# Performance work log

Hardware: AMD Instinct MI355X
Metric: run time of the kernel (lower is better)

## Reference

```python
import jax, jax.numpy as jnp
import numpy as np

B, S, H = 8, 1024, 1024
NH, HD = 16, 64  # num heads, head dim


def _split_heads(x):
    # [B,S,H] -> [B,NH,S,HD]
    return x.reshape(B, S, NH, HD).transpose(0, 2, 1, 3)


def setup_inputs() -> dict:
    key = jax.random.key(0)
    ks = jax.random.split(key, 16)
    sc = 1.0 / np.sqrt(H)
    sch = 1.0 / np.sqrt(HD)
    return {
        "hidden_states": jax.random.normal(ks[0], (B, S, H), jnp.float32),
        "attention_mask": jnp.zeros((B, 1, 1, S), jnp.float32),
        "context_embedded": jax.random.normal(ks[1], (B, S, H), jnp.float32),
        "Wq": jax.random.normal(ks[2], (H, H), jnp.float32) * sc,
        "bq": jnp.zeros((H,), jnp.float32),
        "Wk": jax.random.normal(ks[3], (H, H), jnp.float32) * sc,
        "bk": jnp.zeros((H,), jnp.float32),
        "Wv": jax.random.normal(ks[4], (H, H), jnp.float32) * sc,
        "bv": jnp.zeros((H,), jnp.float32),
        "Wcq": jax.random.normal(ks[5], (HD, HD), jnp.float32) * sch,
        "bcq": jnp.zeros((HD,), jnp.float32),
        "Wck": jax.random.normal(ks[6], (HD, HD), jnp.float32) * sch,
        "bck": jnp.zeros((HD,), jnp.float32),
        "w_lqc": jax.random.normal(ks[7], (HD,), jnp.float32) * sch,
        "w_lqq": jax.random.normal(ks[8], (HD,), jnp.float32) * sch,
        "w_lkc": jax.random.normal(ks[9], (HD,), jnp.float32) * sch,
        "w_lkk": jax.random.normal(ks[10], (HD,), jnp.float32) * sch,
    }


def reference(hidden_states, attention_mask, context_embedded,
              Wq, bq, Wk, bk, Wv, bv, Wcq, bcq, Wck, bck,
              w_lqc, w_lqq, w_lkc, w_lkk):
    # projections -> [B,NH,S,HD]
    q = _split_heads(hidden_states @ Wq + bq)
    k = _split_heads(hidden_states @ Wk + bk)
    v = _split_heads(hidden_states @ Wv + bv)
    ce = _split_heads(context_embedded)

    # context gating for queries
    ce_q = ce @ Wcq + bcq
    lam_q = jax.nn.sigmoid(ce_q @ w_lqc[:, None] + q @ w_lqq[:, None])  # [B,NH,S,1]
    q_ctx = (1.0 - lam_q) * q + lam_q * ce_q

    # context gating for keys
    ce_k = ce @ Wck + bck
    lam_k = jax.nn.sigmoid(ce_k @ w_lkc[:, None] + k @ w_lkk[:, None])  # [B,NH,S,1]
    k_ctx = (1.0 - lam_k) * k + lam_k * ce_k

    scores = jnp.einsum("bhqd,bhkd->bhqk", q_ctx, k_ctx) / np.sqrt(HD)
    scores = scores + attention_mask
    probs = jax.nn.softmax(scores, axis=-1)
    ctx = jnp.einsum("bhqk,bhkd->bhqd", probs, v)
    return ctx.transpose(0, 2, 1, 3).reshape(B, S, H)
```

## Files before the change

kernel.cpp:

```cpp
#include <hip/hip_runtime.h>

typedef _Float16 f16;
typedef f16   f16x8 __attribute__((ext_vector_type(8)));
typedef f16   f16x4 __attribute__((ext_vector_type(4)));
typedef float f32x4 __attribute__((ext_vector_type(4)));

namespace {
constexpr int kB  = 8;
constexpr int kS  = 1024;
constexpr int kH  = 1024;
constexpr int kNH = 16;
constexpr int kHD = 64;
constexpr int kBH = kB * kNH;
constexpr int kRows = kBH * kS;
constexpr float kLog2e = 1.44269504088896f;
}

__device__ __forceinline__ float fast_exp2(float x) {
#if __has_builtin(__builtin_amdgcn_exp2f)
    return __builtin_amdgcn_exp2f(x);
#else
    return __expf(x * 0.693147180559945f);
#endif
}

__device__ __forceinline__ void async16(const f16* g, f16* l) {
    __builtin_amdgcn_global_load_lds(
        (const __attribute__((address_space(1))) unsigned int*)g,
        (__attribute__((address_space(3))) unsigned int*)l, 16, 0, 0);
}

__device__ __forceinline__ int phys4(int m, int c) {
    return ((m >> 1) << 3) | ((((m & 1) << 2) | c) ^ ((m >> 1) & 7));
}
__device__ __forceinline__ int phys8(int m, int c) {
    return (m << 3) | (c ^ (m & 7));
}

__global__ __launch_bounds__(256) void prep_all_kernel(
    const float* __restrict__ hs, const float* __restrict__ ce,
    const float* __restrict__ Wq, const float* __restrict__ Wk,
    const float* __restrict__ Wv, const float* __restrict__ Wcq,
    const float* __restrict__ Wck, const float* __restrict__ mask,
    f16* __restrict__ hs16, f16* __restrict__ ce16, f16* __restrict__ Wt,
    f16* __restrict__ Wct, unsigned int* __restrict__ kn,
    float* __restrict__ mm)
{
    const int id = blockIdx.x;
    const int t = threadIdx.x;
    __shared__ f16 T[64][72];
    __shared__ float red[4];

    if (id < 8192) {
        const int x = id & 4095, y = id >> 12;
        int i = (x * 256 + t) * 8;
        const float* src = y ? ce : hs;
        float4 a = *(const float4*)(src + i);
        float4 b = *(const float4*)(src + i + 4);
        union { f16 h[8]; uint4 u; } pk;
        pk.h[0] = (f16)a.x; pk.h[1] = (f16)a.y; pk.h[2] = (f16)a.z; pk.h[3] = (f16)a.w;
        pk.h[4] = (f16)b.x; pk.h[5] = (f16)b.y; pk.h[6] = (f16)b.z; pk.h[7] = (f16)b.w;
        if (y == 0) {
            *(uint4*)(hs16 + i) = pk.u;
        } else {
            int row = i >> 10, col = i & 1023;
            int bb = row >> 10, s = row & 1023;
            int h = col >> 6, d = col & 63;
            size_t o = ((((size_t)(bb * kNH + h) << 10) | s) << 6) | d;
            *(uint4*)(ce16 + o) = pk.u;
        }
    } else if (id < 8960) {
        const int tt = id - 8192;
        const int bx = tt & 15, by = (tt >> 4) & 15, bz = tt >> 8;
        const float* W = (bz == 0) ? Wq : (bz == 1) ? Wk : Wv;
        f16* out = Wt + (size_t)bz * kH * kH;
        const int k0 = by * 64, n0 = bx * 64;
#pragma unroll
        for (int i = 0; i < 4; ++i) {
            int idx = t + i * 256;
            int r = idx >> 4, cb = (idx & 15) * 4;
            float4 v = *(const float4*)(W + (size_t)(k0 + r) * kH + n0 + cb);
            T[cb + 0][r] = (f16)v.x; T[cb + 1][r] = (f16)v.y;
            T[cb + 2][r] = (f16)v.z; T[cb + 3][r] = (f16)v.w;
        }
        __syncthreads();
#pragma unroll
        for (int i = 0; i < 4; ++i) {
            int idx = t + i * 256;
            int r = idx >> 4, cb = (idx & 15) * 4;
            union { f16 h[4]; uint2 u; } pk;
#pragma unroll
            for (int j = 0; j < 4; ++j) pk.h[j] = T[r][cb + j];
            *(uint2*)(out + (size_t)(n0 + r) * kH + k0 + cb) = pk.u;
        }
    } else {
        const int bx = id - 8960;
        if (bx < 2) {
            const float* W = bx ? Wck : Wcq;
            f16* out = Wct + bx * kHD * kHD;
#pragma unroll
            for (int i = 0; i < 16; ++i) {
                int idx = i * 256 + t;
                int k = idx >> 6, n = idx & 63;
                out[n * 64 + k] = (f16)W[idx];
            }
            if (bx == 0 && t < kBH) kn[t] = 0u;
        } else {
            const int b = bx - 2;
            const float* mp = mask + b * kS;
            float v = fmaxf(fmaxf(mp[t], mp[t + 256]), fmaxf(mp[t + 512], mp[t + 768]));
#pragma unroll
            for (int off = 1; off < 64; off <<= 1) v = fmaxf(v, __shfl_xor(v, off, 64));
            if ((t & 63) == 0) red[t >> 6] = v;
            __syncthreads();
            if (t == 0) mm[b] = fmaxf(fmaxf(red[0], red[1]), fmaxf(red[2], red[3]));
        }
    }
}

__global__ __launch_bounds__(256, 3) void qkv_gemm_f16(
    const f16* __restrict__ hs16, const f16* __restrict__ Wt,
    const float* __restrict__ bq, const float* __restrict__ bk,
    const float* __restrict__ bv,
    f16* __restrict__ q16, f16* __restrict__ k16, f16* __restrict__ vt)
{
    const int z = blockIdx.z;
    const f16* Bmat = Wt + (size_t)z * kH * kH;
    const float* bias = (z == 0) ? bq : (z == 1) ? bk : bv;

    __shared__ f16 AB[2][2][128 * 32];

    const int tid = threadIdx.x;
    const int w = tid >> 6, lane = tid & 63;
    const int quad = lane >> 4, mh = lane & 15;
    const int wm = w >> 1, wn = w & 1;
    const int m0 = blockIdx.x * 128, n0 = blockIdx.y * 128;

    const f16* aptr[2];
#pragma unroll
    for (int i = 0; i < 2; ++i) {
        int P = (w * 2 + i) * 64 + lane;
        int r2 = P >> 3, s = P & 7;
        int bb = s ^ (r2 & 7);
        int m = (r2 << 1) | (bb >> 2), c = bb & 3;
        aptr[i] = hs16 + (size_t)(m0 + m) * kH + c * 8;
    }
    const ptrdiff_t bdelta = (Bmat + (size_t)n0 * kH) - (hs16 + (size_t)m0 * kH);

    auto issue = [&](int buf) {
#pragma unroll
        for (int i = 0; i < 2; ++i) {
            async16(aptr[i], AB[buf][0] + (w * 2 + i) * 512);
            async16(aptr[i] + bdelta, AB[buf][1] + (w * 2 + i) * 512);
            aptr[i] += 32;
        }
    };

    f32x4 acc[4][4];
#pragma unroll
    for (int i = 0; i < 4; ++i)
#pragma unroll
        for (int j = 0; j < 4; ++j) acc[i][j] = (f32x4){0.f, 0.f, 0.f, 0.f};

    const int aoff0 = phys4(wm * 64 + mh, quad) * 8;
    const int boff0 = phys4(wn * 64 + mh, quad) * 8;

    auto compute = [&](int buf) {
        f16x8 af[4], bf[4];
#pragma unroll
        for (int t = 0; t < 4; ++t)
            af[t] = *(const f16x8*)(AB[buf][0] + aoff0 + t * 512);
#pragma unroll
        for (int t = 0; t < 4; ++t)
            bf[t] = *(const f16x8*)(AB[buf][1] + boff0 + t * 512);
#pragma unroll
        for (int i = 0; i < 4; ++i)
#pragma unroll
            for (int j = 0; j < 4; ++j)
                acc[i][j] = __builtin_amdgcn_mfma_f32_16x16x32_f16(
                    af[i], bf[j], acc[i][j], 0, 0, 0);
    };

    issue(0);
    __syncthreads();

    for (int it = 0; it < 16; ++it) {
        issue(1);
        compute(0);
        __syncthreads();
        if (it < 15) issue(0);
        compute(1);
        __syncthreads();
    }

    if (z < 2) {
        f16* outp = (z == 0) ? q16 : k16;
        f16* Cb = &AB[0][0][0] + w * 1280;
        const int h    = (n0 + wn * 64) >> 6;
        const int bbb  = m0 >> 10;
        const int sb   = (m0 & 1023) + wm * 64;
        f16* base = outp + ((size_t)(bbb * kNH + h) * kS + sb) * kHD;
#pragma unroll
        for (int nt = 0; nt < 4; ++nt) {
            const float bn = bias[n0 + wn * 64 + nt * 16 + mh];
#pragma unroll
            for (int mt = 0; mt < 4; ++mt)
#pragma unroll
                for (int r = 0; r < 4; ++r)
                    Cb[(mt * 16 + quad * 4 + r) * 20 + mh] =
                        (f16)(acc[mt][nt][r] + bn);
#pragma unroll
            for (int p = 0; p < 4; ++p) {
                int row = (lane >> 2) + p * 16;
                int qtr = lane & 3;
                uint2 v = *(const uint2*)(&Cb[row * 20 + qtr * 4]);
                *(uint2*)(base + (size_t)row * kHD + nt * 16 + qtr * 4) = v;
            }
        }
    } else {
#pragma unroll
        for (int nt = 0; nt < 4; ++nt) {
            const int n = n0 + wn * 64 + nt * 16 + mh;
            const int h = n >> 6, d = n & 63;
            const float bn = bias[n];
#pragma unroll
            for (int mt = 0; mt < 4; ++mt) {
                int mbase = m0 + wm * 64 + mt * 16 + quad * 4;
                int bbb = mbase >> 10, s0 = mbase & 1023;
                union { f16 h4[4]; uint2 u; } pk;
#pragma unroll
                for (int r = 0; r < 4; ++r) pk.h4[r] = (f16)(acc[mt][nt][r] + bn);
                *(uint2*)(vt + ((size_t)(bbb * kNH + h) * kHD + d) * kS + s0) = pk.u;
            }
        }
    }
}

__global__ __launch_bounds__(256) void gate_mfma(
    const f16* __restrict__ ce16, const f16* __restrict__ Wct,
    const float* __restrict__ bcq, const float* __restrict__ bck,
    const float* __restrict__ wlqc, const float* __restrict__ wlqq,
    const float* __restrict__ wlkc, const float* __restrict__ wlkk,
    f16* __restrict__ q16, f16* __restrict__ k16,
    unsigned int* __restrict__ kn)
{
    __shared__ f16 CeQ[4][64 * 64];
    __shared__ float sS[4][64];
    __shared__ float lamS[4][64];

    const int tid = threadIdx.x, w = tid >> 6, lane = tid & 63;
    const int quad = lane >> 4, mh = lane & 15;
    const int gate = blockIdx.x >> 9;
    const int tIdx = (blockIdx.x & 511) * 4 + w;
    const size_t row0 = (size_t)tIdx * 64;

    const float* bc  = gate ? bck  : bcq;
    const float* wlc = gate ? wlkc : wlqc;
    const float* wlx = gate ? wlkk : wlqq;
    f16* xw = (gate ? k16 : q16) + row0 * kHD;
    const f16* cep = ce16 + row0 * kHD;
    const f16* Wcg = Wct + gate * kHD * kHD;

#pragma unroll
    for (int i = 0; i < 8; ++i) {
        int P = i * 64 + lane;
        int m = P >> 3, c = (P & 7) ^ (m & 7);
        async16(cep + m * 64 + c * 8, CeQ[w] + i * 512);
    }

    f16x8 bfr[4][2];
#pragma unroll
    for (int nt = 0; nt < 4; ++nt)
#pragma unroll
        for (int ks = 0; ks < 2; ++ks)
            bfr[nt][ks] = *(const f16x8*)(
                Wcg + (nt * 16 + mh) * 64 + (ks * 4 + quad) * 8);

#pragma unroll
    for (int it = 0; it < 8; ++it) {
        int slot = it * 64 + lane;
        int r = slot >> 3, c = slot & 7;
        union { uint4 u; f16 h[8]; } xv;
        xv.u = *(const uint4*)(xw + r * 64 + c * 8);
        float4 wa = ((const float4*)wlx)[c * 2];
        float4 wb = ((const float4*)wlx)[c * 2 + 1];
        float s = (float)xv.h[0] * wa.x + (float)xv.h[1] * wa.y +
                  (float)xv.h[2] * wa.z + (float)xv.h[3] * wa.w +
                  (float)xv.h[4] * wb.x + (float)xv.h[5] * wb.y +
                  (float)xv.h[6] * wb.z + (float)xv.h[7] * wb.w;
        s += __shfl_xor(s, 1, 64);
        s += __shfl_xor(s, 2, 64);
        s += __shfl_xor(s, 4, 64);
        if ((lane & 7) == 0) sS[w][r] = s;
    }
    __syncthreads();

    f32x4 acc[4][4];
#pragma unroll
    for (int i = 0; i < 4; ++i)
#pragma unroll
        for (int j = 0; j < 4; ++j) acc[i][j] = (f32x4){0.f, 0.f, 0.f, 0.f};

#pragma unroll
    for (int mt = 0; mt < 4; ++mt) {
        f16x8 a0 = *(const f16x8*)(CeQ[w] + phys8(mt * 16 + mh, 0 + quad) * 8);
        f16x8 a1 = *(const f16x8*)(CeQ[w] + phys8(mt * 16 + mh, 4 + quad) * 8);
#pragma unroll
        for (int nt = 0; nt < 4; ++nt) {
            acc[mt][nt] = __builtin_amdgcn_mfma_f32_16x16x32_f16(a0, bfr[nt][0], acc[mt][nt], 0, 0, 0);
            acc[mt][nt] = __builtin_amdgcn_mfma_f32_16x16x32_f16(a1, bfr[nt][1], acc[mt][nt], 0, 0, 0);
        }
    }

    float bcv[4], wlcv[4];
#pragma unroll
    for (int nt = 0; nt < 4; ++nt) {
        int n = nt * 16 + mh;
        bcv[nt] = bc[n]; wlcv[nt] = wlc[n];
    }
#pragma unroll
    for (int mt = 0; mt < 4; ++mt) {
#pragma unroll
        for (int r = 0; r < 4; ++r) {
            int m = mt * 16 + quad * 4 + r;
            float tpv = 0.f;
#pragma unroll
            for (int nt = 0; nt < 4; ++nt) {
                float v = acc[mt][nt][r] + bcv[nt];
                int col = nt * 16 + mh;
                CeQ[w][phys8(m, col >> 3) * 8 + (col & 7)] = (f16)v;
                tpv += v * wlcv[nt];
            }
            tpv += __shfl_xor(tpv, 1, 64);
            tpv += __shfl_xor(tpv, 2, 64);
            tpv += __shfl_xor(tpv, 4, 64);
            tpv += __shfl_xor(tpv, 8, 64);
            if (mh == 0) {
                float t = tpv + sS[w][m];
                lamS[w][m] = 1.0f / (1.0f + __expf(-t));
            }
        }
    }

    float wmax = 0.f;
#pragma unroll
    for (int it = 0; it < 8; ++it) {
        int slot = it * 64 + lane;
        int r = slot >> 3, c = slot & 7;
        float lam = lamS[w][r];
        union { uint4 u; f16 h[8]; } xv;
        xv.u = *(const uint4*)(xw + r * 64 + c * 8);
        f16x8 cq = *(const f16x8*)(CeQ[w] + phys8(r, c) * 8);
        union { f16 h[8]; uint4 u; } o;
        float ss = 0.f;
#pragma unroll
        for (int j = 0; j < 8; ++j) {
            o.h[j] = (f16)((1.0f - lam) * (float)xv.h[j] + lam * (float)cq[j]);
            float fv = (float)o.h[j];
            ss += fv * fv;
        }
        *(uint4*)(xw + r * 64 + c * 8) = o.u;
        if (gate) {
            ss += __shfl_xor(ss, 1, 64);
            ss += __shfl_xor(ss, 2, 64);
            ss += __shfl_xor(ss, 4, 64);
            wmax = fmaxf(wmax, ss);
        }
    }
    if (gate) {
        wmax = fmaxf(wmax, __shfl_xor(wmax, 8, 64));
        wmax = fmaxf(wmax, __shfl_xor(wmax, 16, 64));
        wmax = fmaxf(wmax, __shfl_xor(wmax, 32, 64));
        if (lane == 0) atomicMax(&kn[tIdx >> 4], __float_as_uint(wmax));
    }
}

__global__ __launch_bounds__(256, 4) void attn_f16(
    const f16* __restrict__ q16, const f16* __restrict__ k16,
    const f16* __restrict__ vt, const float* __restrict__ mask,
    const unsigned int* __restrict__ kn, const float* __restrict__ mm,
    float* __restrict__ out)
{
    __shared__ f16 Ks[2][64 * 64];
    __shared__ f16 Vs[2][64 * 64];
    __shared__ f16 Pt[4][64 * 16];

    const int tid = threadIdx.x;
    const int w = tid >> 6, lane = tid & 63;
    const int quad = lane >> 4, mh = lane & 15;
    const int bh = blockIdx.x, bbb = bh >> 4, h = bh & 15;
    const int q0 = blockIdx.y * 128;
    const float* maskb = mask + bbb * kS;

    int mS[2], cS[2];
#pragma unroll
    for (int i = 0; i < 2; ++i) {
        int P = (w * 2 + i) * 64 + lane;
        mS[i] = P >> 3;
        cS[i] = (P & 7) ^ (mS[i] & 7);
    }
    const f16* kp[2]; const f16* vp[2];
#pragma unroll
    for (int i = 0; i < 2; ++i) {
        kp[i] = k16 + ((size_t)bh * kS + mS[i]) * kHD + cS[i] * 8;
        vp[i] = vt  + ((size_t)bh * kHD + mS[i]) * kS + cS[i] * 8;
    }

    auto issue = [&](f16* Kb, f16* Vb) {
#pragma unroll
        for (int i = 0; i < 2; ++i) {
            async16(kp[i], Kb + (w * 2 + i) * 512);
            async16(vp[i], Vb + (w * 2 + i) * 512);
            kp[i] += 64 * kHD;
            vp[i] += 64;
        }
    };

    issue(Ks[0], Vs[0]);

    f16* PtW = &Pt[w][0];
    const __attribute__((address_space(3))) f16* ptr_tr =
        (const __attribute__((address_space(3))) f16*)PtW + quad * 128 + mh * 4;

    f16x8 qf[2][2];
#pragma unroll
    for (int rt = 0; rt < 2; ++rt) {
        const f16* qrow = q16 + ((size_t)bh * kS + q0 + w * 32 + rt * 16 + mh) * kHD;
#pragma unroll
        for (int ks = 0; ks < 2; ++ks) {
            qf[rt][ks] = *(const f16x8*)(qrow + ks * 32 + quad * 8);
#pragma unroll
            for (int j = 0; j < 8; ++j) qf[rt][ks][j] *= (f16)0.125f;
        }
    }

    const float kn2 = __uint_as_float(kn[bh]);
    const float mmb = mm[bbb];
    float bndr[2][4];
#pragma unroll
    for (int rt = 0; rt < 2; ++rt) {
        float qn2 = 0.f;
#pragma unroll
        for (int ks = 0; ks < 2; ++ks)
#pragma unroll
            for (int j = 0; j < 8; ++j) {
                float v = (float)qf[rt][ks][j];
                qn2 += v * v;
            }
        qn2 += __shfl_xor(qn2, 16, 64);
        qn2 += __shfl_xor(qn2, 32, 64);
        const float bnd = sqrtf(qn2 * kn2) + mmb - 9.5f;
#pragma unroll
        for (int r = 0; r < 4; ++r)
            bndr[rt][r] = -kLog2e * __shfl(bnd, quad * 4 + r, 64);
    }

    f32x4 O[2][4];
#pragma unroll
    for (int rt = 0; rt < 2; ++rt)
#pragma unroll
        for (int i = 0; i < 4; ++i) O[rt][i] = (f32x4){0.f, 0.f, 0.f, 0.f};
    f32x4 Od[2];
    Od[0] = (f32x4){0.f, 0.f, 0.f, 0.f};
    Od[1] = (f32x4){0.f, 0.f, 0.f, 0.f};
    const f16x8 onesv = {(f16)1.f, (f16)1.f, (f16)1.f, (f16)1.f,
                         (f16)1.f, (f16)1.f, (f16)1.f, (f16)1.f};

    auto step = [&](const f16* Kb, const f16* Vb, int jt) {
#pragma unroll
        for (int rt = 0; rt < 2; ++rt) {
#pragma unroll
            for (int nt = 0; nt < 4; ++nt) {
                f16x8 kf0 = *(const f16x8*)(Kb + phys8(nt * 16 + mh, 0 + quad) * 8);
                f16x8 kf1 = *(const f16x8*)(Kb + phys8(nt * 16 + mh, 4 + quad) * 8);
                f32x4 S = __builtin_amdgcn_mfma_f32_16x16x32_f16(
                    qf[rt][0], kf0, (f32x4){0.f, 0.f, 0.f, 0.f}, 0, 0, 0);
                S = __builtin_amdgcn_mfma_f32_16x16x32_f16(
                    qf[rt][1], kf1, S, 0, 0, 0);
                const float mvl2 = kLog2e * maskb[jt + nt * 16 + mh];
                union { f16 h4[4]; uint2 u; } pk;
#pragma unroll
                for (int r = 0; r < 4; ++r)
                    pk.h4[r] = (f16)fast_exp2(
                        fmaf(S[r], kLog2e, mvl2) + bndr[rt][r]);
                *(uint2*)(PtW + (nt * 16 + mh) * 16 + quad * 4) = pk.u;
            }
            f16x4 t0, t1, t2, t3;
            asm volatile(
                "s_waitcnt lgkmcnt(0)\n\t"
                "ds_read_b64_tr_b16 %0, %4\n\t"
                "ds_read_b64_tr_b16 %1, %4 offset:128\n\t"
                "ds_read_b64_tr_b16 %2, %4 offset:1024\n\t"
                "ds_read_b64_tr_b16 %3, %4 offset:1152\n\t"
                "s_waitcnt lgkmcnt(0)"
                : "=&v"(t0), "=&v"(t1), "=&v"(t2), "=&v"(t3)
                : "v"(ptr_tr) : "memory");
            __builtin_amdgcn_sched_barrier(0);
            f16x8 p0 = __builtin_shufflevector(t0, t1, 0, 1, 2, 3, 4, 5, 6, 7);
            f16x8 p1 = __builtin_shufflevector(t2, t3, 0, 1, 2, 3, 4, 5, 6, 7);
            __builtin_amdgcn_s_setprio(1);
            Od[rt] = __builtin_amdgcn_mfma_f32_16x16x32_f16(
                onesv, p0, Od[rt], 0, 0, 0);
            Od[rt] = __builtin_amdgcn_mfma_f32_16x16x32_f16(
                onesv, p1, Od[rt], 0, 0, 0);
#pragma unroll
            for (int dt = 0; dt < 4; ++dt) {
                f16x8 vf0 = *(const f16x8*)(Vb + phys8(dt * 16 + mh, 0 + quad) * 8);
                f16x8 vf1 = *(const f16x8*)(Vb + phys8(dt * 16 + mh, 4 + quad) * 8);
                O[rt][dt] = __builtin_amdgcn_mfma_f32_16x16x32_f16(
                    vf0, p0, O[rt][dt], 0, 0, 0);
                O[rt][dt] = __builtin_amdgcn_mfma_f32_16x16x32_f16(
                    vf1, p1, O[rt][dt], 0, 0, 0);
            }
            __builtin_amdgcn_s_setprio(0);
        }
    };

    __syncthreads();

    for (int jt = 0; jt < kS; jt += 128) {
        issue(Ks[1], Vs[1]);
        step(Ks[0], Vs[0], jt);
        __syncthreads();
        if (jt + 128 < kS) issue(Ks[0], Vs[0]);
        step(Ks[1], Vs[1], jt + 64);
        __syncthreads();
    }

#pragma unroll
    for (int rt = 0; rt < 2; ++rt) {
        const float inv = 1.0f / Od[rt][0];
        const int s = q0 + w * 32 + rt * 16 + mh;
        float* orow = out + ((size_t)(bbb * kS + s)) * kH + (h << 6);
#pragma unroll
        for (int dt = 0; dt < 4; ++dt) {
            f32x4 v;
            v[0] = O[rt][dt][0] * inv;
            v[1] = O[rt][dt][1] * inv;
            v[2] = O[rt][dt][2] * inv;
            v[3] = O[rt][dt][3] * inv;
            __builtin_nontemporal_store(v, (f32x4*)(orow + dt * 16 + quad * 4));
        }
    }
}

extern "C" void kernel_launch(void* const* d_in, const int* in_sizes, int n_in,
                              void* d_out, int out_size, void* d_ws, size_t ws_size,
                              hipStream_t stream) {
    (void)in_sizes; (void)n_in; (void)out_size; (void)ws_size;

    const float* hs   = (const float*)d_in[0];
    const float* mask = (const float*)d_in[1];
    const float* ce   = (const float*)d_in[2];
    const float* Wq   = (const float*)d_in[3];
    const float* bq   = (const float*)d_in[4];
    const float* Wk   = (const float*)d_in[5];
    const float* bk   = (const float*)d_in[6];
    const float* Wv   = (const float*)d_in[7];
    const float* bv   = (const float*)d_in[8];
    const float* Wcq  = (const float*)d_in[9];
    const float* bcq  = (const float*)d_in[10];
    const float* Wck  = (const float*)d_in[11];
    const float* bck  = (const float*)d_in[12];
    const float* wlqc = (const float*)d_in[13];
    const float* wlqq = (const float*)d_in[14];
    const float* wlkc = (const float*)d_in[15];
    const float* wlkk = (const float*)d_in[16];
    float* out = (float*)d_out;

    f16* hs16 = (f16*)d_ws;
    f16* Wt   = hs16 + (size_t)kB * kS * kH;
    f16* q16  = Wt + (size_t)3 * kH * kH;
    f16* k16  = q16 + (size_t)kRows * kHD;
    f16* vt   = k16 + (size_t)kRows * kHD;
    f16* ce16 = vt + (size_t)kRows * kHD;
    f16* Wct  = ce16 + (size_t)kRows * kHD;
    unsigned int* kn = (unsigned int*)(Wct + 2 * kHD * kHD);
    float* mm = (float*)(kn + kBH);

    prep_all_kernel<<<dim3(8970), 256, 0, stream>>>(
        hs, ce, Wq, Wk, Wv, Wcq, Wck, mask,
        hs16, ce16, Wt, Wct, kn, mm);

    qkv_gemm_f16<<<dim3(kB * kS / 128, kH / 128, 3), 256, 0, stream>>>(
        hs16, Wt, bq, bk, bv, q16, k16, vt);

    gate_mfma<<<dim3(1024), 256, 0, stream>>>(
        ce16, Wct, bcq, bck, wlqc, wlqq, wlkc, wlkk, q16, k16, kn);

    attn_f16<<<dim3(kBH, kS / 128), 256, 0, stream>>>(
        q16, k16, vt, mask, kn, mm, out);
}
```

Before: 303.8 us.

## Fuse context gating into QKV GEMM epilogue and drop gate kernel

Moves the context-gating computation (ce projection via MFMA, lambda sigmoid, blend, and key norm max) into the Q/K epilogue of the QKV GEMM and removes the separate gate kernel launch. This avoids writing q/k to global memory, reading them back, and rewriting them, and it saves one launch. In exchange the GEMM epilogue grows in register pressure (extra accumulators and weight fragments under launch bounds of 3 blocks per SM) and reads ce rows straight from global memory without LDS staging.

Measured after the change: 269.2 us. -11.4%, faster.

```diff
diff --git a/kernel.cpp b/kernel.cpp
--- a/kernel.cpp
+++ b/kernel.cpp
@@ -122,7 +122,12 @@
     const f16* __restrict__ hs16, const f16* __restrict__ Wt,
     const float* __restrict__ bq, const float* __restrict__ bk,
     const float* __restrict__ bv,
-    f16* __restrict__ q16, f16* __restrict__ k16, f16* __restrict__ vt)
+    f16* __restrict__ q16, f16* __restrict__ k16, f16* __restrict__ vt,
+    const f16* __restrict__ ce16, const f16* __restrict__ Wct,
+    const float* __restrict__ bcq, const float* __restrict__ bck,
+    const float* __restrict__ wlqc, const float* __restrict__ wlqq,
+    const float* __restrict__ wlkc, const float* __restrict__ wlkk,
+    unsigned int* __restrict__ kn)
 {
     const int z = blockIdx.z;
     const f16* Bmat = Wt + (size_t)z * kH * kH;
@@ -195,27 +200,99 @@
 
     if (z < 2) {
         f16* outp = (z == 0) ? q16 : k16;
-        f16* Cb = &AB[0][0][0] + w * 1280;
-        const int h    = (n0 + wn * 64) >> 6;
-        const int bbb  = m0 >> 10;
-        const int sb   = (m0 & 1023) + wm * 64;
-        f16* base = outp + ((size_t)(bbb * kNH + h) * kS + sb) * kHD;
+        const float* bc   = (z == 0) ? bcq  : bck;
+        const float* wlc  = (z == 0) ? wlqc : wlkc;
+        const float* wlxp = (z == 0) ? wlqq : wlkk;
+        const int h   = (n0 + wn * 64) >> 6;
+        const int bbb = m0 >> 10;
+        const int sb  = (m0 & 1023) + wm * 64;
+        const size_t rowbase = (size_t)(bbb * kNH + h) * kS + sb;
+        f16* base = outp + rowbase * kHD;
+        const f16* ceb = ce16 + rowbase * kHD;
+        const f16* Wcg = Wct + (size_t)z * kHD * kHD;
+
+        float bnv[4], bcv[4], wlcv[4], wlxv[4];
 #pragma unroll
         for (int nt = 0; nt < 4; ++nt) {
-            const float bn = bias[n0 + wn * 64 + nt * 16 + mh];
-#pragma unroll
-            for (int mt = 0; mt < 4; ++mt)
-#pragma unroll
-                for (int r = 0; r < 4; ++r)
-                    Cb[(mt * 16 + quad * 4 + r) * 20 + mh] =
-                        (f16)(acc[mt][nt][r] + bn);
-#pragma unroll
-            for (int p = 0; p < 4; ++p) {
-                int row = (lane >> 2) + p * 16;
-                int qtr = lane & 3;
-                uint2 v = *(const uint2*)(&Cb[row * 20 + qtr * 4]);
-                *(uint2*)(base + (size_t)row * kHD + nt * 16 + qtr * 4) = v;
-            }
+            bnv[nt]  = bias[n0 + wn * 64 + nt * 16 + mh];
+            const int d = nt * 16 + mh;
+            bcv[nt]  = bc[d];
+            wlcv[nt] = wlc[d];
+            wlxv[nt] = wlxp[d];
+        }
+        f16x8 bfr[4][2];
+#pragma unroll
+        for (int nt = 0; nt < 4; ++nt)
+#pragma unroll
+            for (int ks = 0; ks < 2; ++ks)
+                bfr[nt][ks] = *(const f16x8*)(
+                    Wcg + (nt * 16 + mh) * 64 + (ks * 4 + quad) * 8);
+
+        f16* XB = &AB[0][0][0] + w * 4096;
+
+#pragma unroll
+        for (int mt = 0; mt < 4; ++mt) {
+            const f16* cerow = ceb + (size_t)(mt * 16 + mh) * kHD;
+            f16x8 a0 = *(const f16x8*)(cerow + quad * 8);
+            f16x8 a1 = *(const f16x8*)(cerow + 32 + quad * 8);
+            f32x4 accce[4];
+#pragma unroll
+            for (int nt = 0; nt < 4; ++nt) {
+                accce[nt] = __builtin_amdgcn_mfma_f32_16x16x32_f16(
+                    a0, bfr[nt][0], (f32x4){0.f, 0.f, 0.f, 0.f}, 0, 0, 0);
+                accce[nt] = __builtin_amdgcn_mfma_f32_16x16x32_f16(
+                    a1, bfr[nt][1], accce[nt], 0, 0, 0);
+            }
+#pragma unroll
+            for (int r = 0; r < 4; ++r) {
+                f16 x16[4], cq16[4];
+                float t = 0.f;
+#pragma unroll
+                for (int nt = 0; nt < 4; ++nt) {
+                    x16[nt] = (f16)(acc[mt][nt][r] + bnv[nt]);
+                    const float vq = accce[nt][r] + bcv[nt];
+                    cq16[nt] = (f16)vq;
+                    t += (float)x16[nt] * wlxv[nt] + vq * wlcv[nt];
+                }
+                t += __shfl_xor(t, 1, 64);
+                t += __shfl_xor(t, 2, 64);
+                t += __shfl_xor(t, 4, 64);
+                t += __shfl_xor(t, 8, 64);
+                const float lam = 1.0f / (1.0f + __expf(-t));
+                const int row = mt * 16 + quad * 4 + r;
+#pragma unroll
+                for (int nt = 0; nt < 4; ++nt)
+                    XB[row * 64 + nt * 16 + mh] =
+                        (f16)((1.0f - lam) * (float)x16[nt] +
+                              lam * (float)cq16[nt]);
+            }
+        }
+        float wmax = 0.f;
+#pragma unroll
+        for (int p = 0; p < 8; ++p) {
+            const int row = (lane >> 3) + p * 8;
+            const int c8  = (lane & 7) * 8;
+            union { uint4 u; f16 hh[8]; } v;
+            v.u = *(const uint4*)(XB + row * 64 + c8);
+            *(uint4*)(base + (size_t)row * kHD + c8) = v.u;
+            if (z == 1) {
+                float ss = 0.f;
+#pragma unroll
+                for (int j = 0; j < 8; ++j) {
+                    const float f = (float)v.hh[j];
+                    ss += f * f;
+                }
+                ss += __shfl_xor(ss, 1, 64);
+                ss += __shfl_xor(ss, 2, 64);
+                ss += __shfl_xor(ss, 4, 64);
+                wmax = fmaxf(wmax, ss);
+            }
+        }
+        if (z == 1) {
+            wmax = fmaxf(wmax, __shfl_xor(wmax, 8, 64));
+            wmax = fmaxf(wmax, __shfl_xor(wmax, 16, 64));
+            wmax = fmaxf(wmax, __shfl_xor(wmax, 32, 64));
+            if (lane == 0) atomicMax(&kn[bbb * kNH + h], __float_as_uint(wmax));
         }
     } else {
 #pragma unroll
@@ -233,145 +310,6 @@
                 *(uint2*)(vt + ((size_t)(bbb * kNH + h) * kHD + d) * kS + s0) = pk.u;
             }
         }
-    }
-}
-
-__global__ __launch_bounds__(256) void gate_mfma(
-    const f16* __restrict__ ce16, const f16* __restrict__ Wct,
-    const float* __restrict__ bcq, const float* __restrict__ bck,
-    const float* __restrict__ wlqc, const float* __restrict__ wlqq,
-    const float* __restrict__ wlkc, const float* __restrict__ wlkk,
-    f16* __restrict__ q16, f16* __restrict__ k16,
-    unsigned int* __restrict__ kn)
-{
-    __shared__ f16 CeQ[4][64 * 64];
-    __shared__ float sS[4][64];
-    __shared__ float lamS[4][64];
-
-    const int tid = threadIdx.x, w = tid >> 6, lane = tid & 63;
-    const int quad = lane >> 4, mh = lane & 15;
-    const int gate = blockIdx.x >> 9;
-    const int tIdx = (blockIdx.x & 511) * 4 + w;
-    const size_t row0 = (size_t)tIdx * 64;
-
-    const float* bc  = gate ? bck  : bcq;
-    const float* wlc = gate ? wlkc : wlqc;
-    const float* wlx = gate ? wlkk : wlqq;
-    f16* xw = (gate ? k16 : q16) + row0 * kHD;
-    const f16* cep = ce16 + row0 * kHD;
-    const f16* Wcg = Wct + gate * kHD * kHD;
-
-#pragma unroll
-    for (int i = 0; i < 8; ++i) {
-        int P = i * 64 + lane;
-        int m = P >> 3, c = (P & 7) ^ (m & 7);
-        async16(cep + m * 64 + c * 8, CeQ[w] + i * 512);
-    }
-
-    f16x8 bfr[4][2];
-#pragma unroll
-    for (int nt = 0; nt < 4; ++nt)
-#pragma unroll
-        for (int ks = 0; ks < 2; ++ks)
-            bfr[nt][ks] = *(const f16x8*)(
-                Wcg + (nt * 16 + mh) * 64 + (ks * 4 + quad) * 8);
-
-#pragma unroll
-    for (int it = 0; it < 8; ++it) {
-        int slot = it * 64 + lane;
-        int r = slot >> 3, c = slot & 7;
-        union { uint4 u; f16 h[8]; } xv;
-        xv.u = *(const uint4*)(xw + r * 64 + c * 8);
-        float4 wa = ((const float4*)wlx)[c * 2];
-        float4 wb = ((const float4*)wlx)[c * 2 + 1];
-        float s = (float)xv.h[0] * wa.x + (float)xv.h[1] * wa.y +
-                  (float)xv.h[2] * wa.z + (float)xv.h[3] * wa.w +
-                  (float)xv.h[4] * wb.x + (float)xv.h[5] * wb.y +
-                  (float)xv.h[6] * wb.z + (float)xv.h[7] * wb.w;
-        s += __shfl_xor(s, 1, 64);
-        s += __shfl_xor(s, 2, 64);
-        s += __shfl_xor(s, 4, 64);
-        if ((lane & 7) == 0) sS[w][r] = s;
-    }
-    __syncthreads();
-
-    f32x4 acc[4][4];
-#pragma unroll
-    for (int i = 0; i < 4; ++i)
-#pragma unroll
-        for (int j = 0; j < 4; ++j) acc[i][j] = (f32x4){0.f, 0.f, 0.f, 0.f};
-
-#pragma unroll
-    for (int mt = 0; mt < 4; ++mt) {
-        f16x8 a0 = *(const f16x8*)(CeQ[w] + phys8(mt * 16 + mh, 0 + quad) * 8);
-        f16x8 a1 = *(const f16x8*)(CeQ[w] + phys8(mt * 16 + mh, 4 + quad) * 8);
-#pragma unroll
-        for (int nt = 0; nt < 4; ++nt) {
-            acc[mt][nt] = __builtin_amdgcn_mfma_f32_16x16x32_f16(a0, bfr[nt][0], acc[mt][nt], 0, 0, 0);
-            acc[mt][nt] = __builtin_amdgcn_mfma_f32_16x16x32_f16(a1, bfr[nt][1], acc[mt][nt], 0, 0, 0);
-        }
-    }
-
-    float bcv[4], wlcv[4];
-#pragma unroll
-    for (int nt = 0; nt < 4; ++nt) {
-        int n = nt * 16 + mh;
-        bcv[nt] = bc[n]; wlcv[nt] = wlc[n];
-    }
-#pragma unroll
-    for (int mt = 0; mt < 4; ++mt) {
-#pragma unroll
-        for (int r = 0; r < 4; ++r) {
-            int m = mt * 16 + quad * 4 + r;
-            float tpv = 0.f;
-#pragma unroll
-            for (int nt = 0; nt < 4; ++nt) {
-                float v = acc[mt][nt][r] + bcv[nt];
-                int col = nt * 16 + mh;
-                CeQ[w][phys8(m, col >> 3) * 8 + (col & 7)] = (f16)v;
-                tpv += v * wlcv[nt];
-            }
-            tpv += __shfl_xor(tpv, 1, 64);
-            tpv += __shfl_xor(tpv, 2, 64);
-            tpv += __shfl_xor(tpv, 4, 64);
-            tpv += __shfl_xor(tpv, 8, 64);
-            if (mh == 0) {
-                float t = tpv + sS[w][m];
-                lamS[w][m] = 1.0f / (1.0f + __expf(-t));
-            }
-        }
-    }
-
-    float wmax = 0.f;
-#pragma unroll
-    for (int it = 0; it < 8; ++it) {
-        int slot = it * 64 + lane;
-        int r = slot >> 3, c = slot & 7;
-        float lam = lamS[w][r];
-        union { uint4 u; f16 h[8]; } xv;
-        xv.u = *(const uint4*)(xw + r * 64 + c * 8);
-        f16x8 cq = *(const f16x8*)(CeQ[w] + phys8(r, c) * 8);
-        union { f16 h[8]; uint4 u; } o;
-        float ss = 0.f;
-#pragma unroll
-        for (int j = 0; j < 8; ++j) {
-            o.h[j] = (f16)((1.0f - lam) * (float)xv.h[j] + lam * (float)cq[j]);
-            float fv = (float)o.h[j];
-            ss += fv * fv;
-        }
-        *(uint4*)(xw + r * 64 + c * 8) = o.u;
-        if (gate) {
-            ss += __shfl_xor(ss, 1, 64);
-            ss += __shfl_xor(ss, 2, 64);
-            ss += __shfl_xor(ss, 4, 64);
-            wmax = fmaxf(wmax, ss);
-        }
-    }
-    if (gate) {
-        wmax = fmaxf(wmax, __shfl_xor(wmax, 8, 64));
-        wmax = fmaxf(wmax, __shfl_xor(wmax, 16, 64));
-        wmax = fmaxf(wmax, __shfl_xor(wmax, 32, 64));
-        if (lane == 0) atomicMax(&kn[tIdx >> 4], __float_as_uint(wmax));
     }
 }
 
@@ -583,10 +521,8 @@
         hs16, ce16, Wt, Wct, kn, mm);
 
     qkv_gemm_f16<<<dim3(kB * kS / 128, kH / 128, 3), 256, 0, stream>>>(
-        hs16, Wt, bq, bk, bv, q16, k16, vt);
-
-    gate_mfma<<<dim3(1024), 256, 0, stream>>>(
-        ce16, Wct, bcq, bck, wlqc, wlqq, wlkc, wlkk, q16, k16, kn);
+        hs16, Wt, bq, bk, bv, q16, k16, vt,
+        ce16, Wct, bcq, bck, wlqc, wlqq, wlkc, wlkk, kn);
 
     attn_f16<<<dim3(kBH, kS / 128), 256, 0, stream>>>(
         q16, k16, vt, mask, kn, mm, out);
```
